# Performance work log

Measured on AMD Instinct MI355X. Metric: run time of the kernel, lower is better.

Reference implementation:

```python
import jax, jax.numpy as jnp
import numpy as np

EPS = 1e-12  # torch F.normalize default eps


def setup_inputs() -> dict:
    key = jax.random.key(0)
    k1, k2, k3, k4 = jax.random.split(key, 4)
    B, M, D = 4, 8192, 512
    N, P = 128, 1
    x = jax.random.normal(k1, (B, M, D), dtype=jnp.float32)
    phi = jax.random.normal(k2, (D, N, P), dtype=jnp.float32) * (1.0 / D ** 0.5)
    scale = jnp.ones((1,), dtype=jnp.float32)
    W = jax.random.normal(k3, (N, D, D), dtype=jnp.float32) * (1.0 / D ** 0.5)
    b = jax.random.normal(k4, (N, D), dtype=jnp.float32) * 0.01
    return {"x": x, "phi": phi, "scale": scale, "W": W, "b": b}


def _l2norm(v, axis):
    return v / jnp.maximum(jnp.linalg.norm(v, axis=axis, keepdims=True), EPS)


def reference(x, phi, scale, W, b):
    # normalize tokens along feature dim, phi along dim axis, scale phi
    xn = _l2norm(x, axis=2)                      # [B,M,D]
    phin = scale * _l2norm(phi, axis=0)          # [D,N,P]
    logits = jnp.einsum('bmd,dnp->bmnp', xn, phin)
    B, M, N, P = logits.shape
    d = jax.nn.softmax(logits, axis=1)           # dispatch weights (over tokens)
    c = jax.nn.softmax(logits.reshape(B, M, N * P), axis=-1).reshape(B, M, N, P)  # combine (over slots)
    xs = jnp.einsum('bmd,bmnp->bnpd', xn, d)     # slot inputs [B,N,P,D]
    # per-expert Linear, batched over experts (grouped GEMM)
    ys = jnp.einsum('bnpd,nde->bnpe', xs, W) + b[None, :, None, :]
    y = jnp.einsum('bnpd,bmnp->bmd', ys, c)
    return y
```

## Files before the change

### kernel.cpp

```cpp
#include <hip/hip_runtime.h>
#include <math.h>

#define B_ 4
#define M_ 8192
#define D_ 512
#define N_ 128
#define TOK (B_ * M_)
#define MC_ 16
#define MLEN (M_ / MC_)

#define OFF_CS 0
#define OFF_PBT (OFF_CS + 512)
#define OFF_E (OFF_PBT + N_ * D_ / 2)
#define OFF_YST (OFF_E + (size_t)TOK * N_)
#define OFF_XBT (OFF_YST + B_ * D_ * N_ / 2)
#define OFF_EWT (OFF_XBT + (size_t)D_ * TOK / 2)
#define OFF_XP (OFF_EWT + (size_t)N_ * TOK / 2)

typedef __attribute__((ext_vector_type(8))) short s16x8;
typedef __attribute__((ext_vector_type(4))) float f32x4;

__device__ inline short f2bf(float f) {
    union { float f; unsigned u; } v;
    v.f = f;
    unsigned r = v.u + 0x7fffu + ((v.u >> 16) & 1u);
    return (short)(r >> 16);
}

__global__ __launch_bounds__(128) void k_phinorm(const float* __restrict__ phi,
                                                 const float* __restrict__ scale,
                                                 short* __restrict__ pbt) {
    __shared__ float sred[128];
    int n = blockIdx.x, tid = threadIdx.x;
    float ss = 0.f;
    for (int d = tid; d < D_; d += 128) {
        float v = phi[d * N_ + n];
        ss += v * v;
    }
    sred[tid] = ss;
    __syncthreads();
    for (int s = 64; s > 0; s >>= 1) {
        if (tid < s) sred[tid] += sred[tid + s];
        __syncthreads();
    }
    float sc = scale[0] / fmaxf(sqrtf(sred[0]), 1e-12f);
    for (int d = tid; d < D_; d += 128) pbt[n * D_ + d] = f2bf(phi[d * N_ + n] * sc);
}

__global__ __launch_bounds__(512) void k_logits(const float* __restrict__ x,
                                                const short* __restrict__ pbt,
                                                float* __restrict__ E,
                                                short* __restrict__ ewt,
                                                short* __restrict__ xbt,
                                                float* __restrict__ colsum) {
    __shared__ short As[2][128 * 40];
    __shared__ short Bs[2][128 * 40];
    __shared__ float rnS[128];
    short* T = &As[0][0];

    int t = threadIdx.x;
    int r0 = blockIdx.x * 128;
    int sm = t >> 2;
    int kq = (t & 3) * 8;
    const float* xrow = &x[(size_t)(r0 + sm) * D_ + kq];
    const short* brow = &pbt[sm * D_ + kq];
    int wid = t >> 6, lane = t & 63;
    int quad = lane >> 4, l15 = lane & 15;
    int mw = (wid >> 1) * 32, nw = (wid & 1) * 64;
    int dl = t & 31, mg = t >> 5;
    f32x4 acc[2][4] = {};
    float ss = 0.f;

    {
        float4 a0 = *(const float4*)&xrow[0];
        float4 a1 = *(const float4*)&xrow[4];
        s16x8 bv = *(const s16x8*)&brow[0];
        ss += a0.x * a0.x + a0.y * a0.y + a0.z * a0.z + a0.w * a0.w +
              a1.x * a1.x + a1.y * a1.y + a1.z * a1.z + a1.w * a1.w;
        s16x8 av;
        av[0] = f2bf(a0.x); av[1] = f2bf(a0.y); av[2] = f2bf(a0.z); av[3] = f2bf(a0.w);
        av[4] = f2bf(a1.x); av[5] = f2bf(a1.y); av[6] = f2bf(a1.z); av[7] = f2bf(a1.w);
        *(s16x8*)&As[0][sm * 40 + kq] = av;
        *(s16x8*)&Bs[0][sm * 40 + kq] = bv;
    }
    __syncthreads();

#pragma unroll
    for (int kt = 0; kt < 16; kt++) {
        int cur = kt & 1;
        float4 na0, na1;
        s16x8 nbv;
        if (kt < 15) {
            na0 = *(const float4*)&xrow[(kt + 1) * 32];
            na1 = *(const float4*)&xrow[(kt + 1) * 32 + 4];
            nbv = *(const s16x8*)&brow[(kt + 1) * 32];
        }
        s16x8 af[2], bfr[4];
#pragma unroll
        for (int i = 0; i < 2; i++)
            af[i] = *(const s16x8*)&As[cur][(mw + i * 16 + l15) * 40 + quad * 8];
#pragma unroll
        for (int j = 0; j < 4; j++)
            bfr[j] = *(const s16x8*)&Bs[cur][(nw + j * 16 + l15) * 40 + quad * 8];
#pragma unroll
        for (int i = 0; i < 2; i++)
#pragma unroll
            for (int j = 0; j < 4; j++)
                acc[i][j] = __builtin_amdgcn_mfma_f32_16x16x32_bf16(af[i], bfr[j], acc[i][j], 0, 0, 0);
        {
            s16x8 tv;
#pragma unroll
            for (int r = 0; r < 8; r++) tv[r] = As[cur][(mg * 8 + r) * 40 + dl];
            *(s16x8*)&xbt[(size_t)(kt * 32 + dl) * TOK + r0 + mg * 8] = tv;
        }
        if (kt < 15) {
            ss += na0.x * na0.x + na0.y * na0.y + na0.z * na0.z + na0.w * na0.w +
                  na1.x * na1.x + na1.y * na1.y + na1.z * na1.z + na1.w * na1.w;
            s16x8 nav;
            nav[0] = f2bf(na0.x); nav[1] = f2bf(na0.y); nav[2] = f2bf(na0.z); nav[3] = f2bf(na0.w);
            nav[4] = f2bf(na1.x); nav[5] = f2bf(na1.y); nav[6] = f2bf(na1.z); nav[7] = f2bf(na1.w);
            *(s16x8*)&As[cur ^ 1][sm * 40 + kq] = nav;
            *(s16x8*)&Bs[cur ^ 1][sm * 40 + kq] = nbv;
        }
        __syncthreads();
    }
    ss += __shfl_xor(ss, 1, 64);
    ss += __shfl_xor(ss, 2, 64);
    if ((t & 3) == 0) rnS[sm] = 1.0f / fmaxf(sqrtf(ss), 1e-12f);
    __syncthreads();

    int bb = r0 >> 13;
    float rv[2][4];
#pragma unroll
    for (int i = 0; i < 2; i++) {
        int ml = mw + i * 16 + quad * 4;
        rv[i][0] = rnS[ml]; rv[i][1] = rnS[ml + 1];
        rv[i][2] = rnS[ml + 2]; rv[i][3] = rnS[ml + 3];
    }
    short4 ebf[2][4];
#pragma unroll
    for (int j = 0; j < 4; j++) {
        int n = nw + j * 16 + l15;
        float cs = 0.f;
#pragma unroll
        for (int i = 0; i < 2; i++) {
            int mb = r0 + mw + i * 16 + quad * 4;
            f32x4 vv = acc[i][j];
            float e0 = __expf(vv[0] * rv[i][0]), e1 = __expf(vv[1] * rv[i][1]);
            float e2 = __expf(vv[2] * rv[i][2]), e3 = __expf(vv[3] * rv[i][3]);
            cs += e0 + e1 + e2 + e3;
            E[(size_t)(mb + 0) * N_ + n] = e0;
            E[(size_t)(mb + 1) * N_ + n] = e1;
            E[(size_t)(mb + 2) * N_ + n] = e2;
            E[(size_t)(mb + 3) * N_ + n] = e3;
            short4 eb = {f2bf(e0 * rv[i][0]), f2bf(e1 * rv[i][1]),
                         f2bf(e2 * rv[i][2]), f2bf(e3 * rv[i][3])};
            ebf[i][j] = eb;
        }
        cs += __shfl_xor(cs, 16, 64);
        cs += __shfl_xor(cs, 32, 64);
        if (lane < 16) atomicAdd(&colsum[bb * N_ + n], cs);
    }
#pragma unroll
    for (int h = 0; h < 2; h++) {
        if ((wid & 1) == h) {
#pragma unroll
            for (int i = 0; i < 2; i++) {
                int mb = mw + i * 16 + quad * 4;
#pragma unroll
                for (int j = 0; j < 4; j++) {
                    int nl = j * 16 + l15;
                    *(short4*)&T[nl * 136 + mb] = ebf[i][j];
                }
            }
        }
        __syncthreads();
        {
            int nl = t >> 3, c = t & 7;
            s16x8 v0 = *(const s16x8*)&T[nl * 136 + c * 16];
            s16x8 v1 = *(const s16x8*)&T[nl * 136 + c * 16 + 8];
            size_t go = (size_t)(h * 64 + nl) * TOK + r0 + c * 16;
            *(s16x8*)&ewt[go] = v0;
            *(s16x8*)&ewt[go + 8] = v1;
        }
        __syncthreads();
    }
}

__global__ __launch_bounds__(512) void k_xs(const short* __restrict__ ewt,
                                            const short* __restrict__ xbt,
                                            float* __restrict__ part) {
    __shared__ short An[2][128 * 40];
    __shared__ short Bd[2][128 * 40];
    int t = threadIdx.x;
    int bid = blockIdx.x;
    int bi = (bid & 7) * 32 + (bid >> 3);
    int dt = bi & 3, mc = (bi >> 2) & 15, b = bi >> 6;
    int d0 = dt * 128;
    size_t mbase = (size_t)b * M_ + (size_t)mc * MLEN;
    int rs = t >> 2, kq = (t & 3) * 8;
    const short* arow = &ewt[(size_t)rs * TOK + mbase + kq];
    const short* brow = &xbt[(size_t)(d0 + rs) * TOK + mbase + kq];
    int wid = t >> 6, lane = t & 63;
    int quad = lane >> 4, l15 = lane & 15;
    int nw = (wid >> 2) * 64, dw = (wid & 3) * 32;
    f32x4 acc[4][2] = {};

    {
        s16x8 ra = *(const s16x8*)&arow[0];
        s16x8 rb = *(const s16x8*)&brow[0];
        *(s16x8*)&An[0][rs * 40 + kq] = ra;
        *(s16x8*)&Bd[0][rs * 40 + kq] = rb;
    }
    __syncthreads();

#pragma unroll
    for (int kt = 0; kt < 16; kt++) {
        int cur = kt & 1;
        s16x8 ra, rb;
        if (kt < 15) {
            ra = *(const s16x8*)&arow[(kt + 1) * 32];
            rb = *(const s16x8*)&brow[(kt + 1) * 32];
        }
        s16x8 af[4], bf[2];
#pragma unroll
        for (int i = 0; i < 4; i++)
            af[i] = *(const s16x8*)&An[cur][(nw + i * 16 + l15) * 40 + quad * 8];
#pragma unroll
        for (int j = 0; j < 2; j++)
            bf[j] = *(const s16x8*)&Bd[cur][(dw + j * 16 + l15) * 40 + quad * 8];
#pragma unroll
        for (int i = 0; i < 4; i++)
#pragma unroll
            for (int j = 0; j < 2; j++)
                acc[i][j] = __builtin_amdgcn_mfma_f32_16x16x32_bf16(af[i], bf[j], acc[i][j], 0, 0, 0);
        if (kt < 15) {
            *(s16x8*)&An[cur ^ 1][rs * 40 + kq] = ra;
            *(s16x8*)&Bd[cur ^ 1][rs * 40 + kq] = rb;
        }
        __syncthreads();
    }
    size_t pbase = (((size_t)mc * B_ + b) * N_) * D_ + d0;
#pragma unroll
    for (int i = 0; i < 4; i++) {
        int nb = nw + i * 16 + quad * 4;
#pragma unroll
        for (int j = 0; j < 2; j++) {
            int d = dw + j * 16 + l15;
            f32x4 vv = acc[i][j];
            part[pbase + (size_t)(nb + 0) * D_ + d] = vv[0];
            part[pbase + (size_t)(nb + 1) * D_ + d] = vv[1];
            part[pbase + (size_t)(nb + 2) * D_ + d] = vv[2];
            part[pbase + (size_t)(nb + 3) * D_ + d] = vv[3];
        }
    }
}

__global__ __launch_bounds__(256) void k_ys(const float* __restrict__ part,
                                            const float* __restrict__ colsum,
                                            const float* __restrict__ W,
                                            const float* __restrict__ bias,
                                            short* __restrict__ ysT) {
    __shared__ float xsn[B_][D_];
    int bi = blockIdx.x;
    int n = bi >> 2, eq = bi & 3;
    int tid = threadIdx.x;
    {
        int lb = tid >> 6, ld = (tid & 63) * 8;
        float inv = 1.0f / colsum[lb * N_ + n];
        float s0 = 0, s1 = 0, s2 = 0, s3 = 0, s4 = 0, s5 = 0, s6 = 0, s7 = 0;
#pragma unroll
        for (int mc = 0; mc < MC_; mc++) {
            const float* p = &part[(((size_t)mc * B_ + lb) * N_ + n) * D_ + ld];
            float4 v0 = *(const float4*)p;
            float4 v1 = *(const float4*)(p + 4);
            s0 += v0.x; s1 += v0.y; s2 += v0.z; s3 += v0.w;
            s4 += v1.x; s5 += v1.y; s6 += v1.z; s7 += v1.w;
        }
        float4 o0 = {s0 * inv, s1 * inv, s2 * inv, s3 * inv};
        float4 o1 = {s4 * inv, s5 * inv, s6 * inv, s7 * inv};
        *(float4*)&xsn[lb][ld] = o0;
        *(float4*)&xsn[lb][ld + 4] = o1;
    }
    __syncthreads();
    int b = tid >> 6;
    int e = eq * 128 + (tid & 63) * 2;
    const float* Wn = W + (size_t)n * D_ * D_ + e;
    float a0 = 0.f, a1 = 0.f;
#pragma unroll 8
    for (int d = 0; d < D_; d++) {
        float2 w = *(const float2*)&Wn[(size_t)d * D_];
        float xv = xsn[b][d];
        a0 += xv * w.x;
        a1 += xv * w.y;
    }
    float2 bv = *(const float2*)&bias[n * D_ + e];
    ysT[((size_t)b * D_ + e) * N_ + n] = f2bf(a0 + bv.x);
    ysT[((size_t)b * D_ + e + 1) * N_ + n] = f2bf(a1 + bv.y);
}

__global__ __launch_bounds__(256) void k_combine(const float* __restrict__ E,
                                                 const short* __restrict__ ysT,
                                                 float* __restrict__ y) {
    __shared__ short As[128 * 40];
    __shared__ short Bs[128 * 40];
    __shared__ float rsA[2][128];
    __shared__ float rsinv[128];
    int t = threadIdx.x;
    int bid = blockIdx.x;
    int bi = (bid & 7) * 128 + (bid >> 3);
    int dt = bi & 3, mt = bi >> 2;
    int r0 = mt * 128, d0 = dt * 128;
    int bb = r0 >> 13;
    int sm = t >> 1, nh = (t & 1) * 16;
    const float* erow = &E[(size_t)(r0 + sm) * N_ + nh];
    const short* yrow = &ysT[((size_t)bb * D_ + d0 + sm) * N_ + nh];
    int wid = t >> 6, lane = t & 63;
    int quad = lane >> 4, l15 = lane & 15;
    int mw = (wid >> 1) * 64, dw = (wid & 1) * 64;
    f32x4 acc[4][4] = {};
    float rsp = 0.f;

    for (int ks = 0; ks < 4; ks++) {
        int n0 = ks * 32;
        float4 e0 = *(const float4*)&erow[n0];
        float4 e1 = *(const float4*)&erow[n0 + 4];
        float4 e2 = *(const float4*)&erow[n0 + 8];
        float4 e3 = *(const float4*)&erow[n0 + 12];
        rsp += e0.x + e0.y + e0.z + e0.w + e1.x + e1.y + e1.z + e1.w +
               e2.x + e2.y + e2.z + e2.w + e3.x + e3.y + e3.z + e3.w;
        short4 w0 = {f2bf(e0.x), f2bf(e0.y), f2bf(e0.z), f2bf(e0.w)};
        short4 w1 = {f2bf(e1.x), f2bf(e1.y), f2bf(e1.z), f2bf(e1.w)};
        short4 w2 = {f2bf(e2.x), f2bf(e2.y), f2bf(e2.z), f2bf(e2.w)};
        short4 w3 = {f2bf(e3.x), f2bf(e3.y), f2bf(e3.z), f2bf(e3.w)};
        *(short4*)&As[sm * 40 + nh + 0] = w0;
        *(short4*)&As[sm * 40 + nh + 4] = w1;
        *(short4*)&As[sm * 40 + nh + 8] = w2;
        *(short4*)&As[sm * 40 + nh + 12] = w3;
        *(s16x8*)&Bs[sm * 40 + nh] = *(const s16x8*)&yrow[n0];
        *(s16x8*)&Bs[sm * 40 + nh + 8] = *(const s16x8*)&yrow[n0 + 8];
        __syncthreads();
        s16x8 af[4], bf[4];
#pragma unroll
        for (int i = 0; i < 4; i++)
            af[i] = *(const s16x8*)&As[(mw + i * 16 + l15) * 40 + quad * 8];
#pragma unroll
        for (int j = 0; j < 4; j++)
            bf[j] = *(const s16x8*)&Bs[(dw + j * 16 + l15) * 40 + quad * 8];
#pragma unroll
        for (int i = 0; i < 4; i++)
#pragma unroll
            for (int j = 0; j < 4; j++)
                acc[i][j] = __builtin_amdgcn_mfma_f32_16x16x32_bf16(af[i], bf[j], acc[i][j], 0, 0, 0);
        __syncthreads();
    }
    rsA[t & 1][sm] = rsp;
    __syncthreads();
    if (t < 128) rsinv[t] = 1.0f / (rsA[0][t] + rsA[1][t]);
    __syncthreads();
#pragma unroll
    for (int i = 0; i < 4; i++) {
        int mb = mw + i * 16 + quad * 4;
        float i0 = rsinv[mb], i1 = rsinv[mb + 1], i2 = rsinv[mb + 2], i3 = rsinv[mb + 3];
#pragma unroll
        for (int j = 0; j < 4; j++) {
            int d = d0 + dw + j * 16 + l15;
            f32x4 v = acc[i][j];
            y[(size_t)(r0 + mb + 0) * D_ + d] = v[0] * i0;
            y[(size_t)(r0 + mb + 1) * D_ + d] = v[1] * i1;
            y[(size_t)(r0 + mb + 2) * D_ + d] = v[2] * i2;
            y[(size_t)(r0 + mb + 3) * D_ + d] = v[3] * i3;
        }
    }
}

extern "C" void kernel_launch(void* const* d_in, const int* in_sizes, int n_in,
                              void* d_out, int out_size, void* d_ws, size_t ws_size,
                              hipStream_t stream) {
    const float* x = (const float*)d_in[0];
    const float* phi = (const float*)d_in[1];
    const float* scale = (const float*)d_in[2];
    const float* W = (const float*)d_in[3];
    const float* bias = (const float*)d_in[4];
    float* y = (float*)d_out;
    float* ws = (float*)d_ws;

    float* colsum = ws + OFF_CS;
    short* pbt = (short*)(ws + OFF_PBT);
    float* E = ws + OFF_E;
    short* ysT = (short*)(ws + OFF_YST);
    short* xbt = (short*)(ws + OFF_XBT);
    short* ewt = (short*)(ws + OFF_EWT);
    float* part = ws + OFF_XP;

    hipMemsetAsync(colsum, 0, 512 * sizeof(float), stream);

    k_phinorm<<<N_, 128, 0, stream>>>(phi, scale, pbt);
    k_logits<<<TOK / 128, 512, 0, stream>>>(x, pbt, E, ewt, xbt, colsum);
    k_xs<<<B_ * MC_ * 4, 512, 0, stream>>>(ewt, xbt, part);
    k_ys<<<N_ * 4, 256, 0, stream>>>(part, colsum, W, bias, ysT);
    k_combine<<<(TOK / 128) * 4, 256, 0, stream>>>(E, ysT, y);
}
```

Measured before the change: 325.9 us.

## Compute combine softmax in logits kernel and store normalized weights as bf16

The logits kernel now computes per-row softmax sums across the N dimension and writes the combine weights already normalized, as bf16 in row-major layout, instead of a full fp32 exp matrix. k_combine then loads bf16 weights directly, with no row-sum or rescale step, which halves traffic on the largest intermediate. k_ys also splits the D reduction across half-waves with float4 weight loads. The cost is extra shared-memory transposes and syncs in k_logits, and the combine weights are rounded to bf16 after normalization rather than before.

```diff
diff --git a/kernel.cpp b/kernel.cpp
--- a/kernel.cpp
+++ b/kernel.cpp
@@ -11,11 +11,11 @@
 
 #define OFF_CS 0
 #define OFF_PBT (OFF_CS + 512)
-#define OFF_E (OFF_PBT + N_ * D_ / 2)
-#define OFF_YST (OFF_E + (size_t)TOK * N_)
-#define OFF_XBT (OFF_YST + B_ * D_ * N_ / 2)
-#define OFF_EWT (OFF_XBT + (size_t)D_ * TOK / 2)
-#define OFF_XP (OFF_EWT + (size_t)N_ * TOK / 2)
+#define OFF_EBN (OFF_PBT + N_ * D_ / 2)
+#define OFF_EWT (OFF_EBN + (size_t)TOK * N_ / 2)
+#define OFF_XBT (OFF_EWT + (size_t)N_ * TOK / 2)
+#define OFF_YST (OFF_XBT + (size_t)D_ * TOK / 2)
+#define OFF_XP (OFF_YST + B_ * D_ * N_ / 2)
 
 typedef __attribute__((ext_vector_type(8))) short s16x8;
 typedef __attribute__((ext_vector_type(4))) float f32x4;
@@ -49,14 +49,13 @@
 
 __global__ __launch_bounds__(512) void k_logits(const float* __restrict__ x,
                                                 const short* __restrict__ pbt,
-                                                float* __restrict__ E,
+                                                short* __restrict__ ebn,
                                                 short* __restrict__ ewt,
                                                 short* __restrict__ xbt,
                                                 float* __restrict__ colsum) {
-    __shared__ short As[2][128 * 40];
-    __shared__ short Bs[2][128 * 40];
+    __shared__ short smem[4 * 128 * 40];
     __shared__ float rnS[128];
-    short* T = &As[0][0];
+    __shared__ float rsH[2][128];
 
     int t = threadIdx.x;
     int r0 = blockIdx.x * 128;
@@ -80,14 +79,16 @@
         s16x8 av;
         av[0] = f2bf(a0.x); av[1] = f2bf(a0.y); av[2] = f2bf(a0.z); av[3] = f2bf(a0.w);
         av[4] = f2bf(a1.x); av[5] = f2bf(a1.y); av[6] = f2bf(a1.z); av[7] = f2bf(a1.w);
-        *(s16x8*)&As[0][sm * 40 + kq] = av;
-        *(s16x8*)&Bs[0][sm * 40 + kq] = bv;
+        *(s16x8*)&smem[0 * 5120 + sm * 40 + kq] = av;
+        *(s16x8*)&smem[10240 + 0 * 5120 + sm * 40 + kq] = bv;
     }
     __syncthreads();
 
 #pragma unroll
     for (int kt = 0; kt < 16; kt++) {
         int cur = kt & 1;
+        short* As = &smem[cur * 5120];
+        short* Bs = &smem[10240 + cur * 5120];
         float4 na0, na1;
         s16x8 nbv;
         if (kt < 15) {
@@ -98,10 +99,10 @@
         s16x8 af[2], bfr[4];
 #pragma unroll
         for (int i = 0; i < 2; i++)
-            af[i] = *(const s16x8*)&As[cur][(mw + i * 16 + l15) * 40 + quad * 8];
+            af[i] = *(const s16x8*)&As[(mw + i * 16 + l15) * 40 + quad * 8];
 #pragma unroll
         for (int j = 0; j < 4; j++)
-            bfr[j] = *(const s16x8*)&Bs[cur][(nw + j * 16 + l15) * 40 + quad * 8];
+            bfr[j] = *(const s16x8*)&Bs[(nw + j * 16 + l15) * 40 + quad * 8];
 #pragma unroll
         for (int i = 0; i < 2; i++)
 #pragma unroll
@@ -110,7 +111,7 @@
         {
             s16x8 tv;
 #pragma unroll
-            for (int r = 0; r < 8; r++) tv[r] = As[cur][(mg * 8 + r) * 40 + dl];
+            for (int r = 0; r < 8; r++) tv[r] = As[(mg * 8 + r) * 40 + dl];
             *(s16x8*)&xbt[(size_t)(kt * 32 + dl) * TOK + r0 + mg * 8] = tv;
         }
         if (kt < 15) {
@@ -119,8 +120,8 @@
             s16x8 nav;
             nav[0] = f2bf(na0.x); nav[1] = f2bf(na0.y); nav[2] = f2bf(na0.z); nav[3] = f2bf(na0.w);
             nav[4] = f2bf(na1.x); nav[5] = f2bf(na1.y); nav[6] = f2bf(na1.z); nav[7] = f2bf(na1.w);
-            *(s16x8*)&As[cur ^ 1][sm * 40 + kq] = nav;
-            *(s16x8*)&Bs[cur ^ 1][sm * 40 + kq] = nbv;
+            *(s16x8*)&smem[(cur ^ 1) * 5120 + sm * 40 + kq] = nav;
+            *(s16x8*)&smem[10240 + (cur ^ 1) * 5120 + sm * 40 + kq] = nbv;
         }
         __syncthreads();
     }
@@ -137,6 +138,7 @@
         rv[i][0] = rnS[ml]; rv[i][1] = rnS[ml + 1];
         rv[i][2] = rnS[ml + 2]; rv[i][3] = rnS[ml + 3];
     }
+    float rs[2][4] = {};
     short4 ebf[2][4];
 #pragma unroll
     for (int j = 0; j < 4; j++) {
@@ -144,15 +146,12 @@
         float cs = 0.f;
 #pragma unroll
         for (int i = 0; i < 2; i++) {
-            int mb = r0 + mw + i * 16 + quad * 4;
             f32x4 vv = acc[i][j];
             float e0 = __expf(vv[0] * rv[i][0]), e1 = __expf(vv[1] * rv[i][1]);
             float e2 = __expf(vv[2] * rv[i][2]), e3 = __expf(vv[3] * rv[i][3]);
+            acc[i][j][0] = e0; acc[i][j][1] = e1; acc[i][j][2] = e2; acc[i][j][3] = e3;
             cs += e0 + e1 + e2 + e3;
-            E[(size_t)(mb + 0) * N_ + n] = e0;
-            E[(size_t)(mb + 1) * N_ + n] = e1;
-            E[(size_t)(mb + 2) * N_ + n] = e2;
-            E[(size_t)(mb + 3) * N_ + n] = e3;
+            rs[i][0] += e0; rs[i][1] += e1; rs[i][2] += e2; rs[i][3] += e3;
             short4 eb = {f2bf(e0 * rv[i][0]), f2bf(e1 * rv[i][1]),
                          f2bf(e2 * rv[i][2]), f2bf(e3 * rv[i][3])};
             ebf[i][j] = eb;
@@ -161,6 +160,30 @@
         cs += __shfl_xor(cs, 32, 64);
         if (lane < 16) atomicAdd(&colsum[bb * N_ + n], cs);
     }
+#pragma unroll
+    for (int off = 1; off <= 8; off <<= 1)
+#pragma unroll
+        for (int i = 0; i < 2; i++)
+#pragma unroll
+            for (int r = 0; r < 4; r++) rs[i][r] += __shfl_xor(rs[i][r], off, 64);
+    if (l15 == 0) {
+#pragma unroll
+        for (int i = 0; i < 2; i++)
+#pragma unroll
+            for (int r = 0; r < 4; r++)
+                rsH[wid & 1][mw + i * 16 + quad * 4 + r] = rs[i][r];
+    }
+    __syncthreads();
+    float ri[2][4];
+#pragma unroll
+    for (int i = 0; i < 2; i++)
+#pragma unroll
+        for (int r = 0; r < 4; r++) {
+            int m = mw + i * 16 + quad * 4 + r;
+            ri[i][r] = 1.0f / (rsH[0][m] + rsH[1][m]);
+        }
+
+    short* T = smem;
 #pragma unroll
     for (int h = 0; h < 2; h++) {
         if ((wid & 1) == h) {
@@ -184,6 +207,34 @@
             *(s16x8*)&ewt[go + 8] = v1;
         }
         __syncthreads();
+    }
+
+    short* T2 = smem;
+#pragma unroll
+    for (int j = 0; j < 4; j++) {
+        int n = nw + j * 16 + l15;
+#pragma unroll
+        for (int i = 0; i < 2; i++) {
+            int m = mw + i * 16 + quad * 4;
+            f32x4 vv = acc[i][j];
+            T2[(m + 0) * 136 + n] = f2bf(vv[0] * ri[i][0]);
+            T2[(m + 1) * 136 + n] = f2bf(vv[1] * ri[i][1]);
+            T2[(m + 2) * 136 + n] = f2bf(vv[2] * ri[i][2]);
+            T2[(m + 3) * 136 + n] = f2bf(vv[3] * ri[i][3]);
+        }
+    }
+    __syncthreads();
+    {
+        int row = t >> 2, c = (t & 3) * 32;
+        s16x8 v0 = *(const s16x8*)&T2[row * 136 + c];
+        s16x8 v1 = *(const s16x8*)&T2[row * 136 + c + 8];
+        s16x8 v2 = *(const s16x8*)&T2[row * 136 + c + 16];
+        s16x8 v3 = *(const s16x8*)&T2[row * 136 + c + 24];
+        size_t go = (size_t)(r0 + row) * N_ + c;
+        *(s16x8*)&ebn[go] = v0;
+        *(s16x8*)&ebn[go + 8] = v1;
+        *(s16x8*)&ebn[go + 16] = v2;
+        *(s16x8*)&ebn[go + 24] = v3;
     }
 }
 
@@ -284,28 +335,39 @@
     }
     __syncthreads();
     int b = tid >> 6;
-    int e = eq * 128 + (tid & 63) * 2;
+    int lane = tid & 63;
+    int dh = lane >> 5, l32 = lane & 31;
+    int e = eq * 128 + l32 * 4;
     const float* Wn = W + (size_t)n * D_ * D_ + e;
-    float a0 = 0.f, a1 = 0.f;
+    float a0 = 0.f, a1 = 0.f, a2 = 0.f, a3 = 0.f;
+    int dbase = dh * 256;
 #pragma unroll 8
-    for (int d = 0; d < D_; d++) {
-        float2 w = *(const float2*)&Wn[(size_t)d * D_];
+    for (int d = dbase; d < dbase + 256; d++) {
+        float4 w = *(const float4*)&Wn[(size_t)d * D_];
         float xv = xsn[b][d];
         a0 += xv * w.x;
         a1 += xv * w.y;
-    }
-    float2 bv = *(const float2*)&bias[n * D_ + e];
-    ysT[((size_t)b * D_ + e) * N_ + n] = f2bf(a0 + bv.x);
-    ysT[((size_t)b * D_ + e + 1) * N_ + n] = f2bf(a1 + bv.y);
-}
-
-__global__ __launch_bounds__(256) void k_combine(const float* __restrict__ E,
+        a2 += xv * w.z;
+        a3 += xv * w.w;
+    }
+    a0 += __shfl_xor(a0, 32, 64);
+    a1 += __shfl_xor(a1, 32, 64);
+    a2 += __shfl_xor(a2, 32, 64);
+    a3 += __shfl_xor(a3, 32, 64);
+    if (dh == 0) {
+        float4 bv = *(const float4*)&bias[n * D_ + e];
+        ysT[((size_t)b * D_ + e + 0) * N_ + n] = f2bf(a0 + bv.x);
+        ysT[((size_t)b * D_ + e + 1) * N_ + n] = f2bf(a1 + bv.y);
+        ysT[((size_t)b * D_ + e + 2) * N_ + n] = f2bf(a2 + bv.z);
+        ysT[((size_t)b * D_ + e + 3) * N_ + n] = f2bf(a3 + bv.w);
+    }
+}
+
+__global__ __launch_bounds__(256) void k_combine(const short* __restrict__ ebn,
                                                  const short* __restrict__ ysT,
                                                  float* __restrict__ y) {
     __shared__ short As[128 * 40];
     __shared__ short Bs[128 * 40];
-    __shared__ float rsA[2][128];
-    __shared__ float rsinv[128];
     int t = threadIdx.x;
     int bid = blockIdx.x;
     int bi = (bid & 7) * 128 + (bid >> 3);
@@ -313,32 +375,24 @@
     int r0 = mt * 128, d0 = dt * 128;
     int bb = r0 >> 13;
     int sm = t >> 1, nh = (t & 1) * 16;
-    const float* erow = &E[(size_t)(r0 + sm) * N_ + nh];
+    const short* erow = &ebn[(size_t)(r0 + sm) * N_ + nh];
     const short* yrow = &ysT[((size_t)bb * D_ + d0 + sm) * N_ + nh];
     int wid = t >> 6, lane = t & 63;
     int quad = lane >> 4, l15 = lane & 15;
     int mw = (wid >> 1) * 64, dw = (wid & 1) * 64;
     f32x4 acc[4][4] = {};
-    float rsp = 0.f;
-
+
+#pragma unroll
     for (int ks = 0; ks < 4; ks++) {
         int n0 = ks * 32;
-        float4 e0 = *(const float4*)&erow[n0];
-        float4 e1 = *(const float4*)&erow[n0 + 4];
-        float4 e2 = *(const float4*)&erow[n0 + 8];
-        float4 e3 = *(const float4*)&erow[n0 + 12];
-        rsp += e0.x + e0.y + e0.z + e0.w + e1.x + e1.y + e1.z + e1.w +
-               e2.x + e2.y + e2.z + e2.w + e3.x + e3.y + e3.z + e3.w;
-        short4 w0 = {f2bf(e0.x), f2bf(e0.y), f2bf(e0.z), f2bf(e0.w)};
-        short4 w1 = {f2bf(e1.x), f2bf(e1.y), f2bf(e1.z), f2bf(e1.w)};
-        short4 w2 = {f2bf(e2.x), f2bf(e2.y), f2bf(e2.z), f2bf(e2.w)};
-        short4 w3 = {f2bf(e3.x), f2bf(e3.y), f2bf(e3.z), f2bf(e3.w)};
-        *(short4*)&As[sm * 40 + nh + 0] = w0;
-        *(short4*)&As[sm * 40 + nh + 4] = w1;
-        *(short4*)&As[sm * 40 + nh + 8] = w2;
-        *(short4*)&As[sm * 40 + nh + 12] = w3;
-        *(s16x8*)&Bs[sm * 40 + nh] = *(const s16x8*)&yrow[n0];
-        *(s16x8*)&Bs[sm * 40 + nh + 8] = *(const s16x8*)&yrow[n0 + 8];
+        s16x8 ev0 = *(const s16x8*)&erow[n0];
+        s16x8 ev1 = *(const s16x8*)&erow[n0 + 8];
+        s16x8 yv0 = *(const s16x8*)&yrow[n0];
+        s16x8 yv1 = *(const s16x8*)&yrow[n0 + 8];
+        *(s16x8*)&As[sm * 40 + nh] = ev0;
+        *(s16x8*)&As[sm * 40 + nh + 8] = ev1;
+        *(s16x8*)&Bs[sm * 40 + nh] = yv0;
+        *(s16x8*)&Bs[sm * 40 + nh + 8] = yv1;
         __syncthreads();
         s16x8 af[4], bf[4];
 #pragma unroll
@@ -354,22 +408,17 @@
                 acc[i][j] = __builtin_amdgcn_mfma_f32_16x16x32_bf16(af[i], bf[j], acc[i][j], 0, 0, 0);
         __syncthreads();
     }
-    rsA[t & 1][sm] = rsp;
-    __syncthreads();
-    if (t < 128) rsinv[t] = 1.0f / (rsA[0][t] + rsA[1][t]);
-    __syncthreads();
 #pragma unroll
     for (int i = 0; i < 4; i++) {
         int mb = mw + i * 16 + quad * 4;
-        float i0 = rsinv[mb], i1 = rsinv[mb + 1], i2 = rsinv[mb + 2], i3 = rsinv[mb + 3];
 #pragma unroll
         for (int j = 0; j < 4; j++) {
             int d = d0 + dw + j * 16 + l15;
             f32x4 v = acc[i][j];
-            y[(size_t)(r0 + mb + 0) * D_ + d] = v[0] * i0;
-            y[(size_t)(r0 + mb + 1) * D_ + d] = v[1] * i1;
-            y[(size_t)(r0 + mb + 2) * D_ + d] = v[2] * i2;
-            y[(size_t)(r0 + mb + 3) * D_ + d] = v[3] * i3;
+            y[(size_t)(r0 + mb + 0) * D_ + d] = v[0];
+            y[(size_t)(r0 + mb + 1) * D_ + d] = v[1];
+            y[(size_t)(r0 + mb + 2) * D_ + d] = v[2];
+            y[(size_t)(r0 + mb + 3) * D_ + d] = v[3];
         }
     }
 }
@@ -387,17 +436,17 @@
 
     float* colsum = ws + OFF_CS;
     short* pbt = (short*)(ws + OFF_PBT);
-    float* E = ws + OFF_E;
+    short* ebn = (short*)(ws + OFF_EBN);
+    short* ewt = (short*)(ws + OFF_EWT);
+    short* xbt = (short*)(ws + OFF_XBT);
     short* ysT = (short*)(ws + OFF_YST);
-    short* xbt = (short*)(ws + OFF_XBT);
-    short* ewt = (short*)(ws + OFF_EWT);
     float* part = ws + OFF_XP;
 
     hipMemsetAsync(colsum, 0, 512 * sizeof(float), stream);
 
     k_phinorm<<<N_, 128, 0, stream>>>(phi, scale, pbt);
-    k_logits<<<TOK / 128, 512, 0, stream>>>(x, pbt, E, ewt, xbt, colsum);
+    k_logits<<<TOK / 128, 512, 0, stream>>>(x, pbt, ebn, ewt, xbt, colsum);
     k_xs<<<B_ * MC_ * 4, 512, 0, stream>>>(ewt, xbt, part);
     k_ys<<<N_ * 4, 256, 0, stream>>>(part, colsum, W, bias, ysT);
-    k_combine<<<(TOK / 128) * 4, 256, 0, stream>>>(E, ysT, y);
-}
+    k_combine<<<(TOK / 128) * 4, 256, 0, stream>>>(ebn, ysT, y);
+}
```

Result: faster. 311.0 us (-4.6%).
